# Kernel optimization log

Hardware: AMD Instinct MI355X
Metric: run time of the kernel (lower is better)

Reference implementation:

```python
import jax, jax.numpy as jnp
import numpy as np

B, M, D, K = 512, 32, 2048, 3
COUPLING_STRENGTH = 0.1
SPATIAL_DECAY = 2.0


def setup_inputs() -> dict:
    key = jax.random.key(0)
    k1, k2 = jax.random.split(key)
    x = jax.random.normal(k1, (B, M, D), dtype=jnp.float32)  # stacked module activities
    w = jax.random.normal(k2, (D, K), dtype=jnp.float32) * 0.1  # conv1d weight [out=D, in=1, K] squeezed
    return {"x": x, "w": w}


def reference(x, w):
    # x: [B, M, D] stacked module activities; w: [D, K] field-propagation conv weight.
    b, m, d = x.shape
    k = w.shape[1]
    pad = k // 2
    # Conv1d(in=1, out=D, padding=pad) followed by mean over the length dim is
    # exactly: E[b,m,c] = (1/D) * sum_k w[c,k] * S_k, where S_k is the sum of x
    # over the input positions actually touched by tap k (zero padding drops edges).
    T = x.sum(-1)                       # [B, M] total sum
    cs = jnp.cumsum(x, axis=-1)         # [B, M, D] prefix sums
    S_list = []
    for kk in range(k):                 # K is a small static constant
        o = kk - pad                    # tap offset; touched indices [max(0,o), D-1+min(0,o)]
        if o > 0:
            S_list.append(T - cs[..., o - 1])       # drop first o entries
        elif o < 0:
            S_list.append(cs[..., d - 1 + o])       # drop last |o| entries
        else:
            S_list.append(T)
    S = jnp.stack(S_list, axis=-1)      # [B, M, K]
    fields = jnp.einsum('bmk,dk->bmd', S, w) / d  # electric fields [B, M, D]
    # distance-decayed coupling with self-term excluded (i != j in the loop)
    idx = jnp.arange(m)
    decay = jnp.exp(-jnp.abs(idx[:, None] - idx[None, :]).astype(x.dtype) / SPATIAL_DECAY)
    decay = decay * (1.0 - jnp.eye(m, dtype=x.dtype))  # zero diagonal
    weighted = jnp.einsum('ij,bjd->bid', decay, fields)  # [B, M, D]
    return x + COUPLING_STRENGTH * weighted
```

## Files before the change

### kernel.cpp

```cpp
#include <hip/hip_runtime.h>

#define B_ 512
#define M_ 32
#define D_ 2048

__global__ __launch_bounds__(1024) void ephaptic_fused(const float* __restrict__ x,
                                                       const float* __restrict__ w,
                                                       float* __restrict__ out) {
    const int b = blockIdx.x;
    const int tid = threadIdx.x;
    const int m = tid >> 5;
    const int t = tid & 31;

    __shared__ float sT[M_], sF[M_], sL[M_];
    __shared__ float4 sC[M_];

    const size_t rowbase = ((size_t)b * M_ + m) * (size_t)D_;
    const float4* row = (const float4*)(x + rowbase);

    float4 v[16];
    float sum = 0.f;
#pragma unroll
    for (int q = 0; q < 16; ++q) {
        v[q] = row[t + 32 * q];
        sum += (v[q].x + v[q].y) + (v[q].z + v[q].w);
    }
#pragma unroll
    for (int off = 16; off > 0; off >>= 1)
        sum += __shfl_xor(sum, off, 64);
    if (t == 0)  { sT[m] = sum; sF[m] = v[0].x; }
    if (t == 31) { sL[m] = v[15].w; }
    __syncthreads();

    if (tid < M_) {
        const int i = tid;
        float r0 = 0.f, r1 = 0.f, r2 = 0.f;
        for (int j = 0; j < M_; ++j) {
            if (j == i) continue;
            const float dij = __expf(-0.5f * fabsf((float)(i - j)));
            const float T = sT[j];
            r0 += dij * (T - sL[j]);
            r1 += dij * T;
            r2 += dij * (T - sF[j]);
        }
        const float s = 0.1f / (float)D_;
        sC[i] = make_float4(r0 * s, r1 * s, r2 * s, 0.f);
    }
    __syncthreads();

    const float4 co = sC[m];
    const float4* wf = (const float4*)w;
    float4* orow = (float4*)(out + rowbase);
#pragma unroll
    for (int q = 0; q < 16; ++q) {
        const int c4 = t + 32 * q;
        const float4 w0 = wf[c4 * 3 + 0];
        const float4 w1 = wf[c4 * 3 + 1];
        const float4 w2 = wf[c4 * 3 + 2];
        float4 o;
        o.x = v[q].x + co.x * w0.x + co.y * w0.y + co.z * w0.z;
        o.y = v[q].y + co.x * w0.w + co.y * w1.x + co.z * w1.y;
        o.z = v[q].z + co.x * w1.z + co.y * w1.w + co.z * w2.x;
        o.w = v[q].w + co.x * w2.y + co.y * w2.z + co.z * w2.w;
        orow[c4] = o;
    }
}

extern "C" void kernel_launch(void* const* d_in, const int* in_sizes, int n_in,
                              void* d_out, int out_size, void* d_ws, size_t ws_size,
                              hipStream_t stream) {
    const float* x = (const float*)d_in[0];
    const float* w = (const float*)d_in[1];
    float* out = (float*)d_out;
    ephaptic_fused<<<B_, 1024, 0, stream>>>(x, w, out);
}
```

Measured before the change: 55.71 us.

## Split fused kernel into row-sum pass and output pass with smaller blocks

Replaces the single 1024-thread-per-batch kernel with two kernels. The first computes per-row sum, first and last elements into workspace. The second recomputes the coupling coefficients per row via wave shuffles and writes the output. This is meant to raise occupancy and cut register pressure from holding 16 float4s per thread. In exchange, x is read from memory a second time and a kernel launch is added.

Result: slower. 64.18 us (+15.2%).

```diff
diff --git a/kernel.cpp b/kernel.cpp
--- a/kernel.cpp
+++ b/kernel.cpp
@@ -4,64 +4,68 @@
 #define M_ 32
 #define D_ 2048
 
-__global__ __launch_bounds__(1024) void ephaptic_fused(const float* __restrict__ x,
-                                                       const float* __restrict__ w,
-                                                       float* __restrict__ out) {
-    const int b = blockIdx.x;
-    const int tid = threadIdx.x;
-    const int m = tid >> 5;
-    const int t = tid & 31;
+__global__ __launch_bounds__(256) void ephaptic_sums(const float* __restrict__ x,
+                                                     float4* __restrict__ sums) {
+    const int wave = threadIdx.x >> 6;
+    const int lane = threadIdx.x & 63;
+    const int row = blockIdx.x * 4 + wave;
 
-    __shared__ float sT[M_], sF[M_], sL[M_];
-    __shared__ float4 sC[M_];
-
-    const size_t rowbase = ((size_t)b * M_ + m) * (size_t)D_;
-    const float4* row = (const float4*)(x + rowbase);
-
-    float4 v[16];
-    float sum = 0.f;
+    const float4* r4 = (const float4*)(x + (size_t)row * D_);
+    float sum = 0.f, first = 0.f, last = 0.f;
 #pragma unroll
-    for (int q = 0; q < 16; ++q) {
-        v[q] = row[t + 32 * q];
-        sum += (v[q].x + v[q].y) + (v[q].z + v[q].w);
+    for (int q = 0; q < 8; ++q) {
+        float4 v = r4[lane + 64 * q];
+        sum += (v.x + v.y) + (v.z + v.w);
+        if (q == 0) first = v.x;
+        if (q == 7) last = v.w;
     }
 #pragma unroll
-    for (int off = 16; off > 0; off >>= 1)
+    for (int off = 32; off > 0; off >>= 1)
         sum += __shfl_xor(sum, off, 64);
-    if (t == 0)  { sT[m] = sum; sF[m] = v[0].x; }
-    if (t == 31) { sL[m] = v[15].w; }
-    __syncthreads();
+    last = __shfl(last, 63, 64);
+    if (lane == 0) sums[row] = make_float4(sum, first, last, 0.f);
+}
 
-    if (tid < M_) {
-        const int i = tid;
-        float r0 = 0.f, r1 = 0.f, r2 = 0.f;
-        for (int j = 0; j < M_; ++j) {
-            if (j == i) continue;
-            const float dij = __expf(-0.5f * fabsf((float)(i - j)));
-            const float T = sT[j];
-            r0 += dij * (T - sL[j]);
-            r1 += dij * T;
-            r2 += dij * (T - sF[j]);
-        }
-        const float s = 0.1f / (float)D_;
-        sC[i] = make_float4(r0 * s, r1 * s, r2 * s, 0.f);
+__global__ __launch_bounds__(256) void ephaptic_out(const float* __restrict__ x,
+                                                    const float* __restrict__ w,
+                                                    const float4* __restrict__ sums,
+                                                    float* __restrict__ out) {
+    const int row = blockIdx.x;
+    const int b = row >> 5;
+    const int i = row & 31;
+    const int lane = threadIdx.x & 63;
+    const int j = lane & 31;
+
+    const float4 s = sums[b * M_ + j];
+    const float dij = (j == i) ? 0.f : __expf(-0.5f * fabsf((float)(i - j)));
+    float r0 = dij * (s.x - s.z);
+    float r1 = dij * s.x;
+    float r2 = dij * (s.x - s.y);
+#pragma unroll
+    for (int off = 16; off > 0; off >>= 1) {
+        r0 += __shfl_xor(r0, off, 64);
+        r1 += __shfl_xor(r1, off, 64);
+        r2 += __shfl_xor(r2, off, 64);
     }
-    __syncthreads();
+    const float sc = 0.1f / (float)D_;
+    const float c0 = r0 * sc, c1 = r1 * sc, c2 = r2 * sc;
 
-    const float4 co = sC[m];
+    const size_t base = (size_t)row * D_;
+    const float4* xr = (const float4*)(x + base);
+    float4* orow = (float4*)(out + base);
     const float4* wf = (const float4*)w;
-    float4* orow = (float4*)(out + rowbase);
 #pragma unroll
-    for (int q = 0; q < 16; ++q) {
-        const int c4 = t + 32 * q;
+    for (int h = 0; h < 2; ++h) {
+        const int c4 = threadIdx.x + 256 * h;
+        const float4 xv = xr[c4];
         const float4 w0 = wf[c4 * 3 + 0];
         const float4 w1 = wf[c4 * 3 + 1];
         const float4 w2 = wf[c4 * 3 + 2];
         float4 o;
-        o.x = v[q].x + co.x * w0.x + co.y * w0.y + co.z * w0.z;
-        o.y = v[q].y + co.x * w0.w + co.y * w1.x + co.z * w1.y;
-        o.z = v[q].z + co.x * w1.z + co.y * w1.w + co.z * w2.x;
-        o.w = v[q].w + co.x * w2.y + co.y * w2.z + co.z * w2.w;
+        o.x = xv.x + c0 * w0.x + c1 * w0.y + c2 * w0.z;
+        o.y = xv.y + c0 * w0.w + c1 * w1.x + c2 * w1.y;
+        o.z = xv.z + c0 * w1.z + c1 * w1.w + c2 * w2.x;
+        o.w = xv.w + c0 * w2.y + c1 * w2.z + c2 * w2.w;
         orow[c4] = o;
     }
 }
@@ -72,5 +76,8 @@
     const float* x = (const float*)d_in[0];
     const float* w = (const float*)d_in[1];
     float* out = (float*)d_out;
-    ephaptic_fused<<<B_, 1024, 0, stream>>>(x, w, out);
+    float4* sums = (float4*)d_ws;
+
+    ephaptic_sums<<<(B_ * M_) / 4, 256, 0, stream>>>(x, sums);
+    ephaptic_out<<<B_ * M_, 256, 0, stream>>>(x, w, sums, out);
 }
```
